# Performance work log

Measured on AMD Instinct MI355X. Metric: run time of the kernel, lower is better.

Reference implementation:

```python
import jax, jax.numpy as jnp
import numpy as np

N = 20000      # nodes
E = 320000     # edges (before self loops)
D_IN = 256
D_H = 256
D_E = 8
NEG_SLOPE = 0.2


def setup_inputs() -> dict:
    key = jax.random.key(0)
    ks = jax.random.split(key, 12)
    x = jax.random.normal(ks[0], (N, D_IN), jnp.float32)
    edge_index = jax.random.randint(ks[1], (2, E), 0, N, dtype=jnp.int32)
    edge_attr = jax.random.normal(ks[2], (E, D_E), jnp.float32)
    batch = jnp.zeros((N,), jnp.int32)

    def gat_params(k, d_in):
        k1, k2, k3 = jax.random.split(k, 3)
        W = jax.random.normal(k1, (d_in, D_H), jnp.float32) * (1.0 / np.sqrt(d_in))
        a_s = jax.random.normal(k2, (D_H,), jnp.float32) * 0.1
        a_d = jax.random.normal(k3, (D_H,), jnp.float32) * 0.1
        b = jnp.zeros((D_H,), jnp.float32)
        return W, a_s, a_d, b

    W1, as1, ad1, b1 = gat_params(ks[3], D_IN)
    W2, as2, ad2, b2 = gat_params(ks[4], D_H)
    W3, as3, ad3, b3 = gat_params(ks[5], D_H)
    return dict(x=x, edge_index=edge_index, edge_attr=edge_attr, batch=batch,
                W1=W1, as1=as1, ad1=ad1, b1=b1,
                W2=W2, as2=as2, ad2=ad2, b2=b2,
                W3=W3, as3=as3, ad3=ad3, b3=b3)


def gat_conv(x, src, dst, W, a_src, a_dst, b):
    # PyG GATConv, heads=1: h = x W; alpha_e = leakyrelu(<h_src,a_s> + <h_dst,a_d>)
    h = x @ W                                  # [N, D_H]
    s = h @ a_src                              # [N]
    d = h @ a_dst                              # [N]
    alpha = jax.nn.leaky_relu(s[src] + d[dst], NEG_SLOPE)   # [Etot]
    n = h.shape[0]
    m = jax.ops.segment_max(alpha, dst, num_segments=n)     # per-dst max
    ex = jnp.exp(alpha - m[dst])
    denom = jax.ops.segment_sum(ex, dst, num_segments=n)
    w = ex / (denom[dst] + 1e-16)
    out = jax.ops.segment_sum(h[src] * w[:, None], dst, num_segments=n)
    return out + b


def reference(x, edge_index, edge_attr, batch,
              W1, as1, ad1, b1, W2, as2, ad2, b2, W3, as3, ad3, b3):
    # row-normalize input features (zero norms -> 1e-8)
    norms = jnp.linalg.norm(x, axis=1, keepdims=True)
    norms = jnp.where(norms == 0, 1e-8, norms)
    x = x / norms

    # add self loops once (GATConv default add_self_loops=True);
    # edge_attr is ignored since edge_dim=None in GATConv defaults.
    loop = jnp.arange(N, dtype=edge_index.dtype)
    src = jnp.concatenate([edge_index[0], loop])
    dst = jnp.concatenate([edge_index[1], loop])

    x = jax.nn.gelu(gat_conv(x, src, dst, W1, as1, ad1, b1), approximate=False)
    x = jax.nn.gelu(gat_conv(x, src, dst, W2, as2, ad2, b2), approximate=False)
    x = jax.nn.gelu(gat_conv(x, src, dst, W3, as3, ad3, b3), approximate=False)
    return x
```

## Files before the change

### kernel.cpp

```cpp
#include <hip/hip_runtime.h>
#include <math.h>

#define NN 20000
#define EE 320000
#define DD 256
#define ETOT (EE + NN)
#define EDGE_CAP 1544

typedef __attribute__((ext_vector_type(8))) short bf8;
typedef __attribute__((ext_vector_type(4))) float f32x4;

__device__ __forceinline__ float gelu_exact(float x) {
    return 0.5f * x * (1.0f + erff(x * 0.70710678118654752f));
}

__device__ __forceinline__ unsigned short f2bf(float v) {
    unsigned u = __float_as_uint(v);
    u += 0x7fffu + ((u >> 16) & 1u);
    return (unsigned short)(u >> 16);
}
__device__ __forceinline__ float bf2f(unsigned short h) {
    return __uint_as_float(((unsigned)h) << 16);
}
__device__ __forceinline__ void split2(float v, unsigned short& hi, unsigned short& lo) {
    hi = f2bf(v);
    lo = f2bf(v - bf2f(hi));
}

__global__ __launch_bounds__(256) void norm_k(const float* __restrict__ X,
                                              unsigned short* __restrict__ Xh,
                                              unsigned short* __restrict__ Xl,
                                              float* __restrict__ sdZero,
                                              int* __restrict__ deg) {
    int t = threadIdx.x;
    int bid = blockIdx.x;
    if (t < 24) sdZero[bid * 24 + t] = 0.0f;
    if (t >= 32 && t < 36) deg[bid * 4 + (t - 32)] = 1;

    int wave = (bid * 256 + t) >> 6;
    int lane = t & 63;
    const float4 v = *(const float4*)&X[wave * DD + lane * 4];
    float ss = v.x * v.x + v.y * v.y + v.z * v.z + v.w * v.w;
    for (int off = 32; off > 0; off >>= 1) ss += __shfl_down(ss, off, 64);
    ss = __shfl(ss, 0, 64);
    float n = sqrtf(ss);
    if (n == 0.0f) n = 1e-8f;
    float inv = 1.0f / n;
    float o[4] = {v.x * inv, v.y * inv, v.z * inv, v.w * inv};
    ushort4 hv, lv;
    split2(o[0], hv.x, lv.x);
    split2(o[1], hv.y, lv.y);
    split2(o[2], hv.z, lv.z);
    split2(o[3], hv.w, lv.w);
    *(ushort4*)&Xh[wave * DD + lane * 4] = hv;
    *(ushort4*)&Xl[wave * DD + lane * 4] = lv;
}

__global__ __launch_bounds__(256) void splitw_k(const float* __restrict__ W1, const float* __restrict__ W2,
                                                const float* __restrict__ W3, unsigned short* __restrict__ Whl) {
    __shared__ float tile[64][65];
    int t = threadIdx.x;
    int k0 = blockIdx.x * 64;
    int c0 = blockIdx.y * 64;
    int z = blockIdx.z;
    const float* W = (z == 0) ? W1 : (z == 1) ? W2 : W3;
    unsigned short* Wht = Whl + (size_t)z * 2 * DD * DD;
    unsigned short* Wlt = Wht + DD * DD;
#pragma unroll
    for (int i = 0; i < 16; ++i) {
        int idx = t + i * 256;
        int r = idx >> 6, c = idx & 63;
        tile[r][c] = W[(k0 + r) * DD + c0 + c];
    }
    __syncthreads();
#pragma unroll
    for (int i = 0; i < 16; ++i) {
        int idx = t + i * 256;
        int r = idx >> 6, c = idx & 63;
        float v = tile[c][r];
        unsigned short hi, lo;
        split2(v, hi, lo);
        Wht[(c0 + r) * DD + k0 + c] = hi;
        Wlt[(c0 + r) * DD + k0 + c] = lo;
    }
}

__global__ void count_k(const int* __restrict__ ei, int* deg) {
    int e = blockIdx.x * 256 + threadIdx.x;
    if (e < EE) atomicAdd(&deg[ei[EE + e]], 1);
}

#define SCAN_T 1024
#define ITEMS 20
__global__ __launch_bounds__(SCAN_T) void scan_k(const int* __restrict__ deg, int* __restrict__ offs,
                                                 int* __restrict__ cursor, int* __restrict__ csr,
                                                 int* __restrict__ csrD) {
    __shared__ int part[SCAN_T];
    int t = threadIdx.x;
    int base = t * ITEMS;
    int local[ITEMS];
    int sum = 0;
#pragma unroll
    for (int i = 0; i < ITEMS; ++i) {
        int idx = base + i;
        int v = (idx < NN) ? deg[idx] : 0;
        local[i] = v;
        sum += v;
    }
    part[t] = sum;
    __syncthreads();
    for (int s = 1; s < SCAN_T; s <<= 1) {
        int v = (t >= s) ? part[t - s] : 0;
        __syncthreads();
        part[t] += v;
        __syncthreads();
    }
    int run = (t == 0) ? 0 : part[t - 1];
#pragma unroll
    for (int i = 0; i < ITEMS; ++i) {
        int idx = base + i;
        if (idx < NN) {
            offs[idx] = run;
            cursor[idx] = run + 1;
            csr[run] = idx;
            csrD[run] = idx;
            run += local[i];
        }
    }
    if (t == SCAN_T - 1) offs[NN] = part[SCAN_T - 1];
}

__global__ void fill_k(const int* __restrict__ ei, int* cursor, int* __restrict__ csr,
                       int* __restrict__ csrD) {
    int e = blockIdx.x * 256 + threadIdx.x;
    if (e < EE) {
        int s = ei[e];
        int d = ei[EE + e];
        int p = atomicAdd(&cursor[d], 1);
        csr[p] = s;
        csrD[p] = d;
    }
}

__global__ __launch_bounds__(256) void alpha_k(const float* __restrict__ sArr,
                                               const float* __restrict__ dArr,
                                               const int* __restrict__ csr,
                                               const int* __restrict__ csrD,
                                               float* __restrict__ wArr) {
    int p = blockIdx.x * 256 + threadIdx.x;
    if (p < ETOT) {
        float a = sArr[csr[p]] + dArr[csrD[p]];
        a = (a > 0.0f) ? a : 0.2f * a;
        wArr[p] = expf(a);
    }
}

#define LDB 40
__global__ __launch_bounds__(256) void gemm_sd(const unsigned short* __restrict__ Xh,
                                               const unsigned short* __restrict__ Xl,
                                               const unsigned short* __restrict__ Bh,
                                               const unsigned short* __restrict__ Bl,
                                               const float* __restrict__ a_s,
                                               const float* __restrict__ a_d,
                                               float* __restrict__ H,
                                               float* __restrict__ sArr,
                                               float* __restrict__ dArr) {
    __shared__ unsigned short sBh[128 * LDB], sBl[128 * LDB];
    int t = threadIdx.x;
    int m0 = blockIdx.x * 64;
    int n0 = blockIdx.y * 128;
    int w = t >> 6, l = t & 63;
    int rofs = l & 15, kch = l >> 4;

    f32x4 acc[8] = {};

    int c1 = t, c2 = t + 256;
    int br1 = c1 >> 2, bo1 = (c1 & 3) * 8;
    int br2 = c2 >> 2, bo2 = (c2 & 3) * 8;
    const unsigned short* Bh1 = &Bh[(n0 + br1) * DD + bo1];
    const unsigned short* Bh2 = &Bh[(n0 + br2) * DD + bo2];
    const unsigned short* Bl1 = &Bl[(n0 + br1) * DD + bo1];
    const unsigned short* Bl2 = &Bl[(n0 + br2) * DD + bo2];
    bf8 rbh1 = *(const bf8*)Bh1;
    bf8 rbh2 = *(const bf8*)Bh2;
    bf8 rbl1 = *(const bf8*)Bl1;
    bf8 rbl2 = *(const bf8*)Bl2;

    int arow = m0 + w * 16 + rofs;
    bool aval = arow < NN;
    const unsigned short* Ahp = &Xh[(size_t)arow * DD + kch * 8];
    const unsigned short* Alp = &Xl[(size_t)arow * DD + kch * 8];
    bf8 zero = {0, 0, 0, 0, 0, 0, 0, 0};
    bf8 ah = aval ? *(const bf8*)Ahp : zero;
    bf8 al = aval ? *(const bf8*)Alp : zero;

    for (int k0 = 0; k0 < DD; k0 += 32) {
        if (k0) __syncthreads();
        *(bf8*)&sBh[br1 * LDB + bo1] = rbh1;
        *(bf8*)&sBh[br2 * LDB + bo2] = rbh2;
        *(bf8*)&sBl[br1 * LDB + bo1] = rbl1;
        *(bf8*)&sBl[br2 * LDB + bo2] = rbl2;
        __syncthreads();
        int kn = k0 + 32;
        bf8 nah = zero, nal = zero;
        if (kn < DD) {
            rbh1 = *(const bf8*)(Bh1 + kn);
            rbh2 = *(const bf8*)(Bh2 + kn);
            rbl1 = *(const bf8*)(Bl1 + kn);
            rbl2 = *(const bf8*)(Bl2 + kn);
            if (aval) {
                nah = *(const bf8*)(Ahp + kn);
                nal = *(const bf8*)(Alp + kn);
            }
        }
#pragma unroll
        for (int nt = 0; nt < 8; ++nt) {
            int r = nt * 16 + rofs;
            bf8 bh = *(const bf8*)&sBh[r * LDB + kch * 8];
            bf8 bl = *(const bf8*)&sBl[r * LDB + kch * 8];
            acc[nt] = __builtin_amdgcn_mfma_f32_16x16x32_bf16(ah, bh, acc[nt], 0, 0, 0);
            acc[nt] = __builtin_amdgcn_mfma_f32_16x16x32_bf16(ah, bl, acc[nt], 0, 0, 0);
            acc[nt] = __builtin_amdgcn_mfma_f32_16x16x32_bf16(al, bh, acc[nt], 0, 0, 0);
        }
        ah = nah;
        al = nal;
    }
    int row0 = m0 + w * 16 + (l >> 4) * 4;
    int colb = l & 15;
    float sp[4] = {0, 0, 0, 0}, dp[4] = {0, 0, 0, 0};
#pragma unroll
    for (int nt = 0; nt < 8; ++nt) {
        int cc = n0 + nt * 16 + colb;
        float vas = a_s[cc], vad = a_d[cc];
#pragma unroll
        for (int r = 0; r < 4; ++r) {
            int row = row0 + r;
            if (row < NN) H[(size_t)row * DD + cc] = acc[nt][r];
            sp[r] += acc[nt][r] * vas;
            dp[r] += acc[nt][r] * vad;
        }
    }
#pragma unroll
    for (int m = 1; m < 16; m <<= 1) {
#pragma unroll
        for (int r = 0; r < 4; ++r) {
            sp[r] += __shfl_xor(sp[r], m, 64);
            dp[r] += __shfl_xor(dp[r], m, 64);
        }
    }
    if (colb == 0) {
#pragma unroll
        for (int r = 0; r < 4; ++r) {
            int row = row0 + r;
            if (row < NN) {
                atomicAdd(&sArr[row], sp[r]);
                atomicAdd(&dArr[row], dp[r]);
            }
        }
    }
}

__global__ __launch_bounds__(256) void spmm_k(const float* __restrict__ H,
                                              const int* __restrict__ offs,
                                              const int* __restrict__ csr,
                                              const float* __restrict__ wArr,
                                              const float* __restrict__ bias,
                                              unsigned short* __restrict__ Oh,
                                              unsigned short* __restrict__ Ol,
                                              float* __restrict__ outf32) {
    __shared__ float wLds[EDGE_CAP];
    __shared__ int sLds[EDGE_CAP];
    int t = threadIdx.x;
    int sub = t & 7;
    int g = t >> 3;
    int dim = blockIdx.x * 32 + sub * 4;
    const float* Hs = H + dim;
    const float4 bvec = *(const float4*)&bias[dim];

    for (int grp = blockIdx.y; grp < NN / 32; grp += (int)gridDim.y) {
        if (grp != (int)blockIdx.y) __syncthreads();
        int dst0 = grp * 32;
        int dst = dst0 + g;
        int blkBeg = offs[dst0];
        int blkEnd = offs[dst0 + 32];
        int base = blkBeg & ~3;
        int cnt = blkEnd - base;
        for (int i = t * 4; i < cnt; i += 1024) {
            *(float4*)&wLds[i] = *(const float4*)&wArr[base + i];
            *(int4*)&sLds[i] = *(const int4*)&csr[base + i];
        }
        int beg = offs[dst], end = offs[dst + 1];
        __syncthreads();

        float den = 0.0f;
        for (int e = beg + sub; e < end; e += 8) den += wLds[e - base];
        den += __shfl_xor(den, 1, 64);
        den += __shfl_xor(den, 2, 64);
        den += __shfl_xor(den, 4, 64);
        float inv = 1.0f / den;

        float4 A0 = make_float4(0, 0, 0, 0), A1 = A0, A2 = A0, A3 = A0;
        int e = beg - base, lend = end - base;
        for (; e + 3 < lend; e += 4) {
            int s0 = sLds[e], s1 = sLds[e + 1], s2 = sLds[e + 2], s3 = sLds[e + 3];
            float w0 = wLds[e], w1 = wLds[e + 1], w2 = wLds[e + 2], w3 = wLds[e + 3];
            const float4 h0 = *(const float4*)&Hs[(size_t)s0 * DD];
            const float4 h1 = *(const float4*)&Hs[(size_t)s1 * DD];
            const float4 h2 = *(const float4*)&Hs[(size_t)s2 * DD];
            const float4 h3 = *(const float4*)&Hs[(size_t)s3 * DD];
            A0.x += w0 * h0.x; A0.y += w0 * h0.y; A0.z += w0 * h0.z; A0.w += w0 * h0.w;
            A1.x += w1 * h1.x; A1.y += w1 * h1.y; A1.z += w1 * h1.z; A1.w += w1 * h1.w;
            A2.x += w2 * h2.x; A2.y += w2 * h2.y; A2.z += w2 * h2.z; A2.w += w2 * h2.w;
            A3.x += w3 * h3.x; A3.y += w3 * h3.y; A3.z += w3 * h3.z; A3.w += w3 * h3.w;
        }
        for (; e < lend; ++e) {
            int s0 = sLds[e];
            float w0 = wLds[e];
            const float4 h0 = *(const float4*)&Hs[(size_t)s0 * DD];
            A0.x += w0 * h0.x; A0.y += w0 * h0.y; A0.z += w0 * h0.z; A0.w += w0 * h0.w;
        }

        float o0 = gelu_exact((A0.x + A1.x + A2.x + A3.x) * inv + bvec.x);
        float o1 = gelu_exact((A0.y + A1.y + A2.y + A3.y) * inv + bvec.y);
        float o2 = gelu_exact((A0.z + A1.z + A2.z + A3.z) * inv + bvec.z);
        float o3 = gelu_exact((A0.w + A1.w + A2.w + A3.w) * inv + bvec.w);

        ushort4 hv, lv;
        split2(o0, hv.x, lv.x);
        split2(o1, hv.y, lv.y);
        split2(o2, hv.z, lv.z);
        split2(o3, hv.w, lv.w);
        *(ushort4*)&Oh[dst * DD + dim] = hv;
        *(ushort4*)&Ol[dst * DD + dim] = lv;
        if (outf32) {
            float4 o = make_float4(o0, o1, o2, o3);
            *(float4*)&outf32[dst * DD + dim] = o;
        }
    }
}

extern "C" void kernel_launch(void* const* d_in, const int* in_sizes, int n_in,
                              void* d_out, int out_size, void* d_ws, size_t ws_size,
                              hipStream_t stream) {
    const float* x  = (const float*)d_in[0];
    const int* ei   = (const int*)d_in[1];
    const float* W1 = (const float*)d_in[4];
    const float* as1 = (const float*)d_in[5];
    const float* ad1 = (const float*)d_in[6];
    const float* b1 = (const float*)d_in[7];
    const float* W2 = (const float*)d_in[8];
    const float* as2 = (const float*)d_in[9];
    const float* ad2 = (const float*)d_in[10];
    const float* b2 = (const float*)d_in[11];
    const float* W3 = (const float*)d_in[12];
    const float* as3 = (const float*)d_in[13];
    const float* ad3 = (const float*)d_in[14];
    const float* b3 = (const float*)d_in[15];

    float* H = (float*)d_ws;
    unsigned short* Xh = (unsigned short*)(H + (size_t)NN * DD);
    unsigned short* Xl = Xh + (size_t)NN * DD;
    unsigned short* Whl = Xl + (size_t)NN * DD;
    float* sd = (float*)(Whl + (size_t)6 * DD * DD);
    int* offs = (int*)(sd + (size_t)6 * NN);
    int* cursor = offs + (NN + 1);
    int* csr = cursor + NN;
    int* deg = csr + ETOT;
    int* csrD = deg + NN;
    float* wArr = (float*)(csrD + ETOT);

    float* sA1 = sd,           *dA1 = sd + NN;
    float* sA2 = sd + 2 * NN,  *dA2 = sd + 3 * NN;
    float* sA3 = sd + 4 * NN,  *dA3 = sd + 5 * NN;
    unsigned short* Wt1 = Whl;
    unsigned short* Wt2 = Whl + (size_t)2 * DD * DD;
    unsigned short* Wt3 = Whl + (size_t)4 * DD * DD;

    norm_k<<<NN / 4, 256, 0, stream>>>(x, Xh, Xl, sd, deg);
    count_k<<<(EE + 255) / 256, 256, 0, stream>>>(ei, deg);
    scan_k<<<1, SCAN_T, 0, stream>>>(deg, offs, cursor, csr, csrD);
    fill_k<<<(EE + 255) / 256, 256, 0, stream>>>(ei, cursor, csr, csrD);
    splitw_k<<<dim3(4, 4, 3), 256, 0, stream>>>(W1, W2, W3, Whl);

    dim3 ggrid((NN + 63) / 64, DD / 128);
    dim3 sgrid(DD / 32, 313);
    int agrid = (ETOT + 255) / 256;

    gemm_sd<<<ggrid, 256, 0, stream>>>(Xh, Xl, Wt1, Wt1 + DD * DD, as1, ad1, H, sA1, dA1);
    alpha_k<<<agrid, 256, 0, stream>>>(sA1, dA1, csr, csrD, wArr);
    spmm_k<<<sgrid, 256, 0, stream>>>(H, offs, csr, wArr, b1, Xh, Xl, nullptr);
    gemm_sd<<<ggrid, 256, 0, stream>>>(Xh, Xl, Wt2, Wt2 + DD * DD, as2, ad2, H, sA2, dA2);
    alpha_k<<<agrid, 256, 0, stream>>>(sA2, dA2, csr, csrD, wArr);
    spmm_k<<<sgrid, 256, 0, stream>>>(H, offs, csr, wArr, b2, Xh, Xl, nullptr);
    gemm_sd<<<ggrid, 256, 0, stream>>>(Xh, Xl, Wt3, Wt3 + DD * DD, as3, ad3, H, sA3, dA3);
    alpha_k<<<agrid, 256, 0, stream>>>(sA3, dA3, csr, csrD, wArr);
    spmm_k<<<sgrid, 256, 0, stream>>>(H, offs, csr, wArr, b3, Xh, Xl, (float*)d_out);
}
```

Measured before the change: 346.9 us.

## Fold degree scan into first GEMM launch as an extra block column

The single-block prefix scan over node degrees moves into an extra blockIdx.x column of the first gemm_sd launch, using 256 threads instead of 1024, so the scan overlaps the GEMM instead of running as its own serialized launch. The fill_k CSR construction is moved after that GEMM. This saves one kernel launch and hides the latency of the serial scan behind GEMM work. In exchange the scan block does more serial work per thread and reads deg twice, and the extra blocks add slight grid overhead.

```diff
diff --git a/kernel.cpp b/kernel.cpp
--- a/kernel.cpp
+++ b/kernel.cpp
@@ -90,46 +90,6 @@
     if (e < EE) atomicAdd(&deg[ei[EE + e]], 1);
 }
 
-#define SCAN_T 1024
-#define ITEMS 20
-__global__ __launch_bounds__(SCAN_T) void scan_k(const int* __restrict__ deg, int* __restrict__ offs,
-                                                 int* __restrict__ cursor, int* __restrict__ csr,
-                                                 int* __restrict__ csrD) {
-    __shared__ int part[SCAN_T];
-    int t = threadIdx.x;
-    int base = t * ITEMS;
-    int local[ITEMS];
-    int sum = 0;
-#pragma unroll
-    for (int i = 0; i < ITEMS; ++i) {
-        int idx = base + i;
-        int v = (idx < NN) ? deg[idx] : 0;
-        local[i] = v;
-        sum += v;
-    }
-    part[t] = sum;
-    __syncthreads();
-    for (int s = 1; s < SCAN_T; s <<= 1) {
-        int v = (t >= s) ? part[t - s] : 0;
-        __syncthreads();
-        part[t] += v;
-        __syncthreads();
-    }
-    int run = (t == 0) ? 0 : part[t - 1];
-#pragma unroll
-    for (int i = 0; i < ITEMS; ++i) {
-        int idx = base + i;
-        if (idx < NN) {
-            offs[idx] = run;
-            cursor[idx] = run + 1;
-            csr[run] = idx;
-            csrD[run] = idx;
-            run += local[i];
-        }
-    }
-    if (t == SCAN_T - 1) offs[NN] = part[SCAN_T - 1];
-}
-
 __global__ void fill_k(const int* __restrict__ ei, int* cursor, int* __restrict__ csr,
                        int* __restrict__ csrD) {
     int e = blockIdx.x * 256 + threadIdx.x;
@@ -156,6 +116,7 @@
 }
 
 #define LDB 40
+#define GX ((NN + 63) / 64)
 __global__ __launch_bounds__(256) void gemm_sd(const unsigned short* __restrict__ Xh,
                                                const unsigned short* __restrict__ Xl,
                                                const unsigned short* __restrict__ Bh,
@@ -164,8 +125,50 @@
                                                const float* __restrict__ a_d,
                                                float* __restrict__ H,
                                                float* __restrict__ sArr,
-                                               float* __restrict__ dArr) {
+                                               float* __restrict__ dArr,
+                                               const int* __restrict__ deg,
+                                               int* __restrict__ offs,
+                                               int* __restrict__ cursor,
+                                               int* __restrict__ csr,
+                                               int* __restrict__ csrD) {
     __shared__ unsigned short sBh[128 * LDB], sBl[128 * LDB];
+
+    if (blockIdx.x >= GX) {
+        if (blockIdx.y == 0) {
+            int* part = (int*)sBh;
+            int t = threadIdx.x;
+            const int IT = (NN + 255) / 256;
+            int base = t * IT;
+            int sum = 0;
+            for (int i = 0; i < IT; ++i) {
+                int idx = base + i;
+                if (idx < NN) sum += deg[idx];
+            }
+            part[t] = sum;
+            __syncthreads();
+            for (int s = 1; s < 256; s <<= 1) {
+                int v = (t >= s) ? part[t - s] : 0;
+                __syncthreads();
+                part[t] += v;
+                __syncthreads();
+            }
+            int run = (t == 0) ? 0 : part[t - 1];
+            for (int i = 0; i < IT; ++i) {
+                int idx = base + i;
+                if (idx < NN) {
+                    int dv = deg[idx];
+                    offs[idx] = run;
+                    cursor[idx] = run + 1;
+                    csr[run] = idx;
+                    csrD[run] = idx;
+                    run += dv;
+                }
+            }
+            if (t == 255) offs[NN] = part[255];
+        }
+        return;
+    }
+
     int t = threadIdx.x;
     int m0 = blockIdx.x * 64;
     int n0 = blockIdx.y * 128;
@@ -378,21 +381,24 @@
 
     norm_k<<<NN / 4, 256, 0, stream>>>(x, Xh, Xl, sd, deg);
     count_k<<<(EE + 255) / 256, 256, 0, stream>>>(ei, deg);
-    scan_k<<<1, SCAN_T, 0, stream>>>(deg, offs, cursor, csr, csrD);
-    fill_k<<<(EE + 255) / 256, 256, 0, stream>>>(ei, cursor, csr, csrD);
     splitw_k<<<dim3(4, 4, 3), 256, 0, stream>>>(W1, W2, W3, Whl);
 
-    dim3 ggrid((NN + 63) / 64, DD / 128);
+    dim3 ggrid1(GX + 1, DD / 128);
+    dim3 ggrid(GX, DD / 128);
     dim3 sgrid(DD / 32, 313);
     int agrid = (ETOT + 255) / 256;
 
-    gemm_sd<<<ggrid, 256, 0, stream>>>(Xh, Xl, Wt1, Wt1 + DD * DD, as1, ad1, H, sA1, dA1);
+    gemm_sd<<<ggrid1, 256, 0, stream>>>(Xh, Xl, Wt1, Wt1 + DD * DD, as1, ad1, H, sA1, dA1,
+                                        deg, offs, cursor, csr, csrD);
+    fill_k<<<(EE + 255) / 256, 256, 0, stream>>>(ei, cursor, csr, csrD);
     alpha_k<<<agrid, 256, 0, stream>>>(sA1, dA1, csr, csrD, wArr);
     spmm_k<<<sgrid, 256, 0, stream>>>(H, offs, csr, wArr, b1, Xh, Xl, nullptr);
-    gemm_sd<<<ggrid, 256, 0, stream>>>(Xh, Xl, Wt2, Wt2 + DD * DD, as2, ad2, H, sA2, dA2);
+    gemm_sd<<<ggrid, 256, 0, stream>>>(Xh, Xl, Wt2, Wt2 + DD * DD, as2, ad2, H, sA2, dA2,
+                                       nullptr, nullptr, nullptr, nullptr, nullptr);
     alpha_k<<<agrid, 256, 0, stream>>>(sA2, dA2, csr, csrD, wArr);
     spmm_k<<<sgrid, 256, 0, stream>>>(H, offs, csr, wArr, b2, Xh, Xl, nullptr);
-    gemm_sd<<<ggrid, 256, 0, stream>>>(Xh, Xl, Wt3, Wt3 + DD * DD, as3, ad3, H, sA3, dA3);
+    gemm_sd<<<ggrid, 256, 0, stream>>>(Xh, Xl, Wt3, Wt3 + DD * DD, as3, ad3, H, sA3, dA3,
+                                       nullptr, nullptr, nullptr, nullptr, nullptr);
     alpha_k<<<agrid, 256, 0, stream>>>(sA3, dA3, csr, csrD, wArr);
     spmm_k<<<sgrid, 256, 0, stream>>>(H, offs, csr, wArr, b3, Xh, Xl, (float*)d_out);
 }
```

Result: slower. 367.3 us (+5.9%).
